# Performance work log

Hardware: AMD Instinct MI355X
Metric: run time of the kernel (lower is better)

## Reference

```python
import jax, jax.numpy as jnp
import numpy as np

B, N, E, H = 16, 1024, 128, 8  # batch, num_patches, emb_dim, num_heads
INNER = E * H                   # inner_dim = emb_dim * num_heads = 1024
LN_EPS = 1e-5
NEG_MAX = jnp.finfo(jnp.float32).max  # module uses -finfo.max on the diagonal


def setup_inputs() -> dict:
    key = jax.random.key(0)
    k0, k1, k2 = jax.random.split(key, 3)
    x = jax.random.normal(k0, (B, N, E), dtype=jnp.float32)
    ln_w = jnp.ones((E,), jnp.float32)
    ln_b = jnp.zeros((E,), jnp.float32)
    w_qkv = jax.random.normal(k1, (E, 3 * INNER), jnp.float32) * (E ** -0.5)
    scale = jnp.full((H,), E ** -0.5, jnp.float32)  # learnable per-head LSA scale
    w_proj = jax.random.normal(k2, (INNER, E), jnp.float32) * (INNER ** -0.5)
    b_proj = jnp.zeros((E,), jnp.float32)
    return {"x": x, "ln_w": ln_w, "ln_b": ln_b, "w_qkv": w_qkv,
            "scale": scale, "w_proj": w_proj, "b_proj": b_proj}


def reference(x, ln_w, ln_b, w_qkv, scale, w_proj, b_proj):
    # LayerNorm over emb_dim
    mu = jnp.mean(x, axis=-1, keepdims=True)
    var = jnp.mean(jnp.square(x - mu), axis=-1, keepdims=True)
    xn = (x - mu) * jax.lax.rsqrt(var + LN_EPS) * ln_w + ln_b

    # QKV projection (no bias), chunk into q,k,v of [B,N,INNER]
    qkv = xn @ w_qkv
    q, k, v = jnp.split(qkv, 3, axis=-1)

    # 'b n (h d) -> b h n d' with h = H, d = E
    def to_heads(t):
        return t.reshape(B, N, H, E).transpose(0, 2, 1, 3)
    q, k, v = to_heads(q), to_heads(k), to_heads(v)

    # per-head learnable scale (LSA), then mask diagonal to -max
    dots = jnp.einsum("bhnd,bhmd->bhnm", q, k) * scale[None, :, None, None]
    idx = jnp.arange(N)
    dots = dots.at[:, :, idx, idx].set(-NEG_MAX)

    attn = jax.nn.softmax(dots, axis=-1)  # dropout p=0.0 -> identity
    out = jnp.einsum("bhnm,bhmd->bhnd", attn, v)

    # 'b h n d -> b n (h d)', then output projection (with bias)
    out = out.transpose(0, 2, 1, 3).reshape(B, N, INNER)
    return out @ w_proj + b_proj
```

## Files before the change

### kernel.cpp

```cpp
#include <hip/hip_runtime.h>
#include <hip/hip_bf16.h>

typedef __bf16 bf16x8 __attribute__((ext_vector_type(8)));
typedef float f32x4 __attribute__((ext_vector_type(4)));

__device__ __forceinline__ unsigned short f2bf(float f) {
  union { __hip_bfloat16 h; unsigned short u; } cv;
  cv.h = __float2bfloat16(f);
  return cv.u;
}

__device__ __forceinline__ bf16x8 ld_frag(const unsigned short* p) {
  bf16x8 v;
  __builtin_memcpy(&v, __builtin_assume_aligned(p, 16), 16);
  return v;
}
__device__ __forceinline__ uint4 ld16(const unsigned short* p) {
  uint4 v;
  __builtin_memcpy(&v, __builtin_assume_aligned(p, 16), 16);
  return v;
}
__device__ __forceinline__ void st16(unsigned short* p, uint4 v) {
  __builtin_memcpy(__builtin_assume_aligned(p, 16), &v, 16);
}

__global__ __launch_bounds__(256) void ln_kernel(const float* __restrict__ x,
                                                 const float* __restrict__ w,
                                                 const float* __restrict__ b,
                                                 unsigned short* __restrict__ xn) {
  int wave = threadIdx.x >> 6;
  int lane = threadIdx.x & 63;
  int row = blockIdx.x * 4 + wave;
  const float* xr = x + (size_t)row * 128;
  float2 v = *reinterpret_cast<const float2*>(xr + lane * 2);
  float s1 = v.x + v.y;
  float s2 = v.x * v.x + v.y * v.y;
#pragma unroll
  for (int off = 32; off > 0; off >>= 1) {
    s1 += __shfl_xor(s1, off, 64);
    s2 += __shfl_xor(s2, off, 64);
  }
  float mu = s1 * (1.0f / 128.0f);
  float var = s2 * (1.0f / 128.0f) - mu * mu;
  float rstd = rsqrtf(var + 1e-5f);
  float a0 = (v.x - mu) * rstd * w[lane * 2] + b[lane * 2];
  float a1 = (v.y - mu) * rstd * w[lane * 2 + 1] + b[lane * 2 + 1];
  unsigned int pk = (unsigned int)f2bf(a0) | ((unsigned int)f2bf(a1) << 16);
  *reinterpret_cast<unsigned int*>(xn + (size_t)row * 128 + lane * 2) = pk;
}

__global__ __launch_bounds__(256) void tcast_kernel(const float* __restrict__ in,
                                                    unsigned short* __restrict__ out,
                                                    int R, int C) {
  __shared__ float tile[32][33];
  int tx = threadIdx.x & 31, ty = threadIdx.x >> 5;
  int c0 = blockIdx.x * 32, r0 = blockIdx.y * 32;
#pragma unroll
  for (int k = 0; k < 4; k++)
    tile[ty + 8 * k][tx] = in[(size_t)(r0 + ty + 8 * k) * C + c0 + tx];
  __syncthreads();
#pragma unroll
  for (int k = 0; k < 4; k++)
    out[(size_t)(c0 + ty + 8 * k) * R + r0 + tx] = f2bf(tile[tx][ty + 8 * k]);
}

__global__ __launch_bounds__(256) void qkv_gemm(const unsigned short* __restrict__ A,
                                                const unsigned short* __restrict__ Bt,
                                                unsigned short* __restrict__ qk,
                                                unsigned short* __restrict__ Vt) {
  __shared__ unsigned short Al[64 * 136];
  __shared__ unsigned short Bl[128 * 136];
  int t = threadIdx.x;
  int i0 = blockIdx.x * 64, c0 = blockIdx.y * 128;
  int l = t & 15, rr = t >> 4;
#pragma unroll
  for (int p = 0; p < 4; p++) {
    int r = rr + 16 * p;
    st16(&Al[r * 136 + l * 8], ld16(&A[(size_t)(i0 + r) * 128 + l * 8]));
  }
#pragma unroll
  for (int p = 0; p < 8; p++) {
    int r = rr + 16 * p;
    st16(&Bl[r * 136 + l * 8], ld16(&Bt[(size_t)(c0 + r) * 128 + l * 8]));
  }
  __syncthreads();
  int w = t >> 6, lane = t & 63, l15 = lane & 15, quad = lane >> 4;
  int wy = (w >> 1) * 32, wx = (w & 1) * 64;
  const f32x4 fz = {0.f, 0.f, 0.f, 0.f};
  f32x4 acc[2][4];
#pragma unroll
  for (int i = 0; i < 2; i++)
#pragma unroll
    for (int j = 0; j < 4; j++) acc[i][j] = fz;
#pragma unroll
  for (int ks = 0; ks < 4; ks++) {
    bf16x8 af[2], bfr[4];
#pragma unroll
    for (int i = 0; i < 2; i++)
      af[i] = ld_frag(&Al[(wy + 16 * i + l15) * 136 + 32 * ks + quad * 8]);
#pragma unroll
    for (int j = 0; j < 4; j++)
      bfr[j] = ld_frag(&Bl[(wx + 16 * j + l15) * 136 + 32 * ks + quad * 8]);
#pragma unroll
    for (int i = 0; i < 2; i++)
#pragma unroll
      for (int j = 0; j < 4; j++)
        acc[i][j] = __builtin_amdgcn_mfma_f32_16x16x32_bf16(af[i], bfr[j], acc[i][j], 0, 0, 0);
  }
  if (blockIdx.y < 16) {
#pragma unroll
    for (int i = 0; i < 2; i++)
#pragma unroll
      for (int j = 0; j < 4; j++)
#pragma unroll
        for (int r = 0; r < 4; r++) {
          int row = i0 + wy + 16 * i + quad * 4 + r;
          int col = c0 + wx + 16 * j + l15;
          qk[(size_t)row * 2048 + col] = f2bf(acc[i][j][r]);
        }
  } else {
    int vc0 = (blockIdx.y - 16) * 128;
#pragma unroll
    for (int i = 0; i < 2; i++)
#pragma unroll
      for (int j = 0; j < 4; j++) {
        int vcol = vc0 + wx + 16 * j + l15;
        int hh = vcol >> 7, dd = vcol & 127;
        int row0 = i0 + wy + 16 * i + quad * 4;
        int bb = row0 >> 10, nn = row0 & 1023;
        ushort4 pk;
        pk.x = f2bf(acc[i][j][0]); pk.y = f2bf(acc[i][j][1]);
        pk.z = f2bf(acc[i][j][2]); pk.w = f2bf(acc[i][j][3]);
        *reinterpret_cast<ushort4*>(Vt + (size_t)(bb * 8 + hh) * 131072 +
                                    (size_t)dd * 1024 + nn) = pk;
      }
  }
}

__global__ __launch_bounds__(256, 3) void attn_kernel(const unsigned short* __restrict__ qk,
                                                      const unsigned short* __restrict__ Vt,
                                                      const float* __restrict__ scale,
                                                      unsigned short* __restrict__ aout) {
  __shared__ unsigned short Kl[64 * 136];
  __shared__ unsigned short Vl[128 * 72];
  __shared__ unsigned short Pl[128 * 72];
  int t = threadIdx.x;
  int idx = blockIdx.x;
  int bh = idx & 127, qt = idx >> 7;
  int b = bh >> 3, h = bh & 7;
  int q0 = qt * 128;
  float sc = scale[h];
  int w = t >> 6, lane = t & 63, l15 = lane & 15, quad = lane >> 4;

  bf16x8 qf[2][4];
#pragma unroll
  for (int g = 0; g < 2; g++) {
    const unsigned short* qp =
        qk + (size_t)(b * 1024 + q0 + 32 * w + 16 * g + l15) * 2048 + h * 128;
#pragma unroll
    for (int ks = 0; ks < 4; ks++) qf[g][ks] = ld_frag(qp + 32 * ks + quad * 8);
  }
  const f32x4 fz = {0.f, 0.f, 0.f, 0.f};
  f32x4 o[2][8];
#pragma unroll
  for (int g = 0; g < 2; g++)
#pragma unroll
    for (int i = 0; i < 8; i++) o[g][i] = fz;
  float plsum[2][4];
#pragma unroll
  for (int g = 0; g < 2; g++)
#pragma unroll
    for (int r = 0; r < 4; r++) plsum[g][r] = 0.f;

  const unsigned short* kbase = qk + (size_t)b * 1024 * 2048 + 1024 + h * 128;
  const unsigned short* vbase = Vt + (size_t)bh * 131072;
  int lk = t & 15, rrk = t >> 4;
  int lv = t & 7, rrv = t >> 3;

  for (int kt = 0; kt < 16; kt++) {
    int k0 = kt * 64;
    uint4 kreg[4], vreg[4];
#pragma unroll
    for (int p = 0; p < 4; p++)
      kreg[p] = ld16(kbase + (size_t)(k0 + rrk + 16 * p) * 2048 + lk * 8);
#pragma unroll
    for (int p = 0; p < 4; p++)
      vreg[p] = ld16(vbase + (size_t)(rrv + 32 * p) * 1024 + k0 + lv * 8);
    __syncthreads();
#pragma unroll
    for (int p = 0; p < 4; p++) st16(&Kl[(rrk + 16 * p) * 136 + lk * 8], kreg[p]);
#pragma unroll
    for (int p = 0; p < 4; p++) st16(&Vl[(rrv + 32 * p) * 72 + lv * 8], vreg[p]);
    __syncthreads();

#pragma unroll
    for (int ct = 0; ct < 4; ct++) {
      f32x4 acc0 = fz, acc1 = fz;
#pragma unroll
      for (int ks = 0; ks < 4; ks++) {
        bf16x8 kf = ld_frag(&Kl[(16 * ct + l15) * 136 + 32 * ks + quad * 8]);
        acc0 = __builtin_amdgcn_mfma_f32_16x16x32_bf16(qf[0][ks], kf, acc0, 0, 0, 0);
        acc1 = __builtin_amdgcn_mfma_f32_16x16x32_bf16(qf[1][ks], kf, acc1, 0, 0, 0);
      }
#pragma unroll
      for (int g = 0; g < 2; g++) {
        f32x4 a = g ? acc1 : acc0;
        bool dj = (q0 + 32 * w + 16 * g) == (k0 + 16 * ct);
#pragma unroll
        for (int r = 0; r < 4; r++) {
          float p = __expf(a[r] * sc);
          if (dj && (quad * 4 + r) == l15) p = 0.f;
          plsum[g][r] += p;
          Pl[(32 * w + 16 * g + quad * 4 + r) * 72 + 16 * ct + l15] = f2bf(p);
        }
      }
    }
    __syncthreads();

    bf16x8 pa[2][2];
#pragma unroll
    for (int g = 0; g < 2; g++)
#pragma unroll
      for (int ks2 = 0; ks2 < 2; ks2++)
        pa[g][ks2] = ld_frag(&Pl[(32 * w + 16 * g + l15) * 72 + 32 * ks2 + quad * 8]);
#pragma unroll
    for (int c8 = 0; c8 < 8; c8++) {
#pragma unroll
      for (int ks2 = 0; ks2 < 2; ks2++) {
        bf16x8 vf = ld_frag(&Vl[(16 * c8 + l15) * 72 + 32 * ks2 + quad * 8]);
        o[0][c8] = __builtin_amdgcn_mfma_f32_16x16x32_bf16(pa[0][ks2], vf, o[0][c8], 0, 0, 0);
        o[1][c8] = __builtin_amdgcn_mfma_f32_16x16x32_bf16(pa[1][ks2], vf, o[1][c8], 0, 0, 0);
      }
    }
  }

#pragma unroll
  for (int g = 0; g < 2; g++)
#pragma unroll
    for (int r = 0; r < 4; r++) {
      float s = plsum[g][r];
#pragma unroll
      for (int off = 1; off < 16; off <<= 1) s += __shfl_xor(s, off, 64);
      float rl = 1.0f / s;
      int row = b * 1024 + q0 + 32 * w + 16 * g + quad * 4 + r;
#pragma unroll
      for (int c8 = 0; c8 < 8; c8++) {
        int col = h * 128 + 16 * c8 + l15;
        aout[(size_t)row * 1024 + col] = f2bf(o[g][c8][r] * rl);
      }
    }
}

__global__ __launch_bounds__(256) void proj_gemm(const unsigned short* __restrict__ A,
                                                 const unsigned short* __restrict__ Bt,
                                                 const float* __restrict__ bias,
                                                 float* __restrict__ out) {
  __shared__ unsigned short Al[64 * 136];
  __shared__ unsigned short Bl[128 * 136];
  int t = threadIdx.x;
  int i0 = blockIdx.x * 64;
  int w = t >> 6, lane = t & 63, l15 = lane & 15, quad = lane >> 4;
  int wy = (w >> 1) * 32, wx = (w & 1) * 64;
  const f32x4 fz = {0.f, 0.f, 0.f, 0.f};
  f32x4 acc[2][4];
#pragma unroll
  for (int i = 0; i < 2; i++)
#pragma unroll
    for (int j = 0; j < 4; j++) acc[i][j] = fz;
  int l = t & 15, rr = t >> 4;
  for (int kb = 0; kb < 8; kb++) {
    int k0 = kb * 128;
    uint4 areg[4], breg[8];
#pragma unroll
    for (int p = 0; p < 4; p++)
      areg[p] = ld16(&A[(size_t)(i0 + rr + 16 * p) * 1024 + k0 + l * 8]);
#pragma unroll
    for (int p = 0; p < 8; p++)
      breg[p] = ld16(&Bt[(size_t)(rr + 16 * p) * 1024 + k0 + l * 8]);
    __syncthreads();
#pragma unroll
    for (int p = 0; p < 4; p++) st16(&Al[(rr + 16 * p) * 136 + l * 8], areg[p]);
#pragma unroll
    for (int p = 0; p < 8; p++) st16(&Bl[(rr + 16 * p) * 136 + l * 8], breg[p]);
    __syncthreads();
#pragma unroll
    for (int ks = 0; ks < 4; ks++) {
      bf16x8 af[2], bfr[4];
#pragma unroll
      for (int i = 0; i < 2; i++)
        af[i] = ld_frag(&Al[(wy + 16 * i + l15) * 136 + 32 * ks + quad * 8]);
#pragma unroll
      for (int j = 0; j < 4; j++)
        bfr[j] = ld_frag(&Bl[(wx + 16 * j + l15) * 136 + 32 * ks + quad * 8]);
#pragma unroll
      for (int i = 0; i < 2; i++)
#pragma unroll
        for (int j = 0; j < 4; j++)
          acc[i][j] = __builtin_amdgcn_mfma_f32_16x16x32_bf16(af[i], bfr[j], acc[i][j], 0, 0, 0);
    }
  }
#pragma unroll
  for (int i = 0; i < 2; i++)
#pragma unroll
    for (int j = 0; j < 4; j++) {
      int col = wx + 16 * j + l15;
      float bv = bias[col];
#pragma unroll
      for (int r = 0; r < 4; r++) {
        int row = i0 + wy + 16 * i + quad * 4 + r;
        out[(size_t)row * 128 + col] = acc[i][j][r] + bv;
      }
    }
}

extern "C" void kernel_launch(void* const* d_in, const int* in_sizes, int n_in,
                              void* d_out, int out_size, void* d_ws, size_t ws_size,
                              hipStream_t stream) {
  const float* x      = (const float*)d_in[0];
  const float* ln_w   = (const float*)d_in[1];
  const float* ln_b   = (const float*)d_in[2];
  const float* w_qkv  = (const float*)d_in[3];
  const float* scale  = (const float*)d_in[4];
  const float* w_proj = (const float*)d_in[5];
  const float* b_proj = (const float*)d_in[6];
  float* out = (float*)d_out;

  char* ws = (char*)d_ws;
  unsigned short* xn     = (unsigned short*)(ws);
  unsigned short* wqkvT  = (unsigned short*)(ws + 4194304);
  unsigned short* wprojT = (unsigned short*)(ws + 4980736);
  unsigned short* qk     = (unsigned short*)(ws + 5242880);
  unsigned short* Vt     = (unsigned short*)(ws + 72351744);
  unsigned short* aout   = (unsigned short*)(ws + 105906176);

  ln_kernel<<<dim3(4096), dim3(256), 0, stream>>>(x, ln_w, ln_b, xn);
  tcast_kernel<<<dim3(96, 4), dim3(256), 0, stream>>>(w_qkv, wqkvT, 128, 3072);
  tcast_kernel<<<dim3(4, 32), dim3(256), 0, stream>>>(w_proj, wprojT, 1024, 128);
  qkv_gemm<<<dim3(256, 24), dim3(256), 0, stream>>>(xn, wqkvT, qk, Vt);
  attn_kernel<<<dim3(1024), dim3(256), 0, stream>>>(qk, Vt, scale, aout);
  proj_gemm<<<dim3(256), dim3(256), 0, stream>>>(aout, wprojT, b_proj, out);
}
```

Baseline: 216.1 us.

## Retile QKV, attention and projection kernels; read K/V fragments directly from global

The QKV GEMM moves to 128x128 tiles with K split into two 64-wide LDS stages. The attention kernel now processes 256 queries per block, 64 per wave, and drops the shared K/V staging and block-wide barriers. Each wave loads K and V MFMA fragments straight from global or L2 and writes P into its own swizzled LDS slice. The projection GEMM is split into two 64-column halves to double the grid. Together these aim for more reuse per block and less synchronisation, at the cost of higher register pressure, lower occupancy (launch bound 2) and uncoalesced-looking global fragment loads.

```diff
diff --git a/kernel.cpp b/kernel.cpp
--- a/kernel.cpp
+++ b/kernel.cpp
@@ -68,48 +68,55 @@
                                                 const unsigned short* __restrict__ Bt,
                                                 unsigned short* __restrict__ qk,
                                                 unsigned short* __restrict__ Vt) {
-  __shared__ unsigned short Al[64 * 136];
-  __shared__ unsigned short Bl[128 * 136];
+  __shared__ unsigned short Al[128 * 72];
+  __shared__ unsigned short Bl[128 * 72];
   int t = threadIdx.x;
-  int i0 = blockIdx.x * 64, c0 = blockIdx.y * 128;
-  int l = t & 15, rr = t >> 4;
-#pragma unroll
-  for (int p = 0; p < 4; p++) {
-    int r = rr + 16 * p;
-    st16(&Al[r * 136 + l * 8], ld16(&A[(size_t)(i0 + r) * 128 + l * 8]));
-  }
-#pragma unroll
-  for (int p = 0; p < 8; p++) {
-    int r = rr + 16 * p;
-    st16(&Bl[r * 136 + l * 8], ld16(&Bt[(size_t)(c0 + r) * 128 + l * 8]));
-  }
-  __syncthreads();
+  int i0 = blockIdx.x * 128, c0 = blockIdx.y * 128;
+  int lg = t & 7, rr = t >> 3;
   int w = t >> 6, lane = t & 63, l15 = lane & 15, quad = lane >> 4;
-  int wy = (w >> 1) * 32, wx = (w & 1) * 64;
+  int wy = (w >> 1) * 64, wx = (w & 1) * 64;
   const f32x4 fz = {0.f, 0.f, 0.f, 0.f};
-  f32x4 acc[2][4];
-#pragma unroll
-  for (int i = 0; i < 2; i++)
+  f32x4 acc[4][4];
+#pragma unroll
+  for (int i = 0; i < 4; i++)
 #pragma unroll
     for (int j = 0; j < 4; j++) acc[i][j] = fz;
-#pragma unroll
-  for (int ks = 0; ks < 4; ks++) {
-    bf16x8 af[2], bfr[4];
-#pragma unroll
-    for (int i = 0; i < 2; i++)
-      af[i] = ld_frag(&Al[(wy + 16 * i + l15) * 136 + 32 * ks + quad * 8]);
-#pragma unroll
-    for (int j = 0; j < 4; j++)
-      bfr[j] = ld_frag(&Bl[(wx + 16 * j + l15) * 136 + 32 * ks + quad * 8]);
-#pragma unroll
-    for (int i = 0; i < 2; i++)
+
+#pragma unroll
+  for (int kt = 0; kt < 2; kt++) {
+    int k0 = kt * 64;
+    uint4 areg[4], breg[4];
+#pragma unroll
+    for (int p = 0; p < 4; p++)
+      areg[p] = ld16(&A[(size_t)(i0 + rr + 32 * p) * 128 + k0 + lg * 8]);
+#pragma unroll
+    for (int p = 0; p < 4; p++)
+      breg[p] = ld16(&Bt[(size_t)(c0 + rr + 32 * p) * 128 + k0 + lg * 8]);
+    __syncthreads();
+#pragma unroll
+    for (int p = 0; p < 4; p++) st16(&Al[(rr + 32 * p) * 72 + lg * 8], areg[p]);
+#pragma unroll
+    for (int p = 0; p < 4; p++) st16(&Bl[(rr + 32 * p) * 72 + lg * 8], breg[p]);
+    __syncthreads();
+#pragma unroll
+    for (int ks = 0; ks < 2; ks++) {
+      bf16x8 af[4], bfr[4];
+#pragma unroll
+      for (int i = 0; i < 4; i++)
+        af[i] = ld_frag(&Al[(wy + 16 * i + l15) * 72 + 32 * ks + quad * 8]);
 #pragma unroll
       for (int j = 0; j < 4; j++)
-        acc[i][j] = __builtin_amdgcn_mfma_f32_16x16x32_bf16(af[i], bfr[j], acc[i][j], 0, 0, 0);
+        bfr[j] = ld_frag(&Bl[(wx + 16 * j + l15) * 72 + 32 * ks + quad * 8]);
+#pragma unroll
+      for (int i = 0; i < 4; i++)
+#pragma unroll
+        for (int j = 0; j < 4; j++)
+          acc[i][j] = __builtin_amdgcn_mfma_f32_16x16x32_bf16(af[i], bfr[j], acc[i][j], 0, 0, 0);
+    }
   }
   if (blockIdx.y < 16) {
 #pragma unroll
-    for (int i = 0; i < 2; i++)
+    for (int i = 0; i < 4; i++)
 #pragma unroll
       for (int j = 0; j < 4; j++)
 #pragma unroll
@@ -121,7 +128,7 @@
   } else {
     int vc0 = (blockIdx.y - 16) * 128;
 #pragma unroll
-    for (int i = 0; i < 2; i++)
+    for (int i = 0; i < 4; i++)
 #pragma unroll
       for (int j = 0; j < 4; j++) {
         int vcol = vc0 + wx + 16 * j + l15;
@@ -137,112 +144,100 @@
   }
 }
 
-__global__ __launch_bounds__(256, 3) void attn_kernel(const unsigned short* __restrict__ qk,
+__global__ __launch_bounds__(256, 2) void attn_kernel(const unsigned short* __restrict__ qk,
                                                       const unsigned short* __restrict__ Vt,
                                                       const float* __restrict__ scale,
                                                       unsigned short* __restrict__ aout) {
-  __shared__ unsigned short Kl[64 * 136];
-  __shared__ unsigned short Vl[128 * 72];
-  __shared__ unsigned short Pl[128 * 72];
+  __shared__ unsigned short Pl[256 * 72];
   int t = threadIdx.x;
   int idx = blockIdx.x;
   int bh = idx & 127, qt = idx >> 7;
   int b = bh >> 3, h = bh & 7;
-  int q0 = qt * 128;
+  int q0 = qt * 256;
   float sc = scale[h];
   int w = t >> 6, lane = t & 63, l15 = lane & 15, quad = lane >> 4;
 
-  bf16x8 qf[2][4];
-#pragma unroll
-  for (int g = 0; g < 2; g++) {
-    const unsigned short* qp =
-        qk + (size_t)(b * 1024 + q0 + 32 * w + 16 * g + l15) * 2048 + h * 128;
-#pragma unroll
-    for (int ks = 0; ks < 4; ks++) qf[g][ks] = ld_frag(qp + 32 * ks + quad * 8);
+  bf16x8 qf[4][4];
+  {
+    const unsigned short* qb = qk + (size_t)(b * 1024) * 2048 + h * 128;
+#pragma unroll
+    for (int g = 0; g < 4; g++) {
+      const unsigned short* qp = qb + (size_t)(q0 + 64 * w + 16 * g + l15) * 2048;
+#pragma unroll
+      for (int ks = 0; ks < 4; ks++) qf[g][ks] = ld_frag(qp + 32 * ks + quad * 8);
+    }
   }
   const f32x4 fz = {0.f, 0.f, 0.f, 0.f};
-  f32x4 o[2][8];
-#pragma unroll
-  for (int g = 0; g < 2; g++)
+  f32x4 o[4][8];
+#pragma unroll
+  for (int g = 0; g < 4; g++)
 #pragma unroll
     for (int i = 0; i < 8; i++) o[g][i] = fz;
-  float plsum[2][4];
-#pragma unroll
-  for (int g = 0; g < 2; g++)
+  float plsum[4][4];
+#pragma unroll
+  for (int g = 0; g < 4; g++)
 #pragma unroll
     for (int r = 0; r < 4; r++) plsum[g][r] = 0.f;
 
-  const unsigned short* kbase = qk + (size_t)b * 1024 * 2048 + 1024 + h * 128;
+  const unsigned short* kbase = qk + (size_t)(b * 1024) * 2048 + 1024 + h * 128;
   const unsigned short* vbase = Vt + (size_t)bh * 131072;
-  int lk = t & 15, rrk = t >> 4;
-  int lv = t & 7, rrv = t >> 3;
+  unsigned short* Pw = &Pl[(64 * w) * 72];
+  int rswz = (l15 >> 2) << 1;
+  int wgoff = ((2 * 0) + 0, 0);
+  (void)wgoff;
 
   for (int kt = 0; kt < 16; kt++) {
     int k0 = kt * 64;
-    uint4 kreg[4], vreg[4];
-#pragma unroll
-    for (int p = 0; p < 4; p++)
-      kreg[p] = ld16(kbase + (size_t)(k0 + rrk + 16 * p) * 2048 + lk * 8);
-#pragma unroll
-    for (int p = 0; p < 4; p++)
-      vreg[p] = ld16(vbase + (size_t)(rrv + 32 * p) * 1024 + k0 + lv * 8);
-    __syncthreads();
-#pragma unroll
-    for (int p = 0; p < 4; p++) st16(&Kl[(rrk + 16 * p) * 136 + lk * 8], kreg[p]);
-#pragma unroll
-    for (int p = 0; p < 4; p++) st16(&Vl[(rrv + 32 * p) * 72 + lv * 8], vreg[p]);
-    __syncthreads();
-
 #pragma unroll
     for (int ct = 0; ct < 4; ct++) {
-      f32x4 acc0 = fz, acc1 = fz;
+      f32x4 acc[4] = {fz, fz, fz, fz};
 #pragma unroll
       for (int ks = 0; ks < 4; ks++) {
-        bf16x8 kf = ld_frag(&Kl[(16 * ct + l15) * 136 + 32 * ks + quad * 8]);
-        acc0 = __builtin_amdgcn_mfma_f32_16x16x32_bf16(qf[0][ks], kf, acc0, 0, 0, 0);
-        acc1 = __builtin_amdgcn_mfma_f32_16x16x32_bf16(qf[1][ks], kf, acc1, 0, 0, 0);
-      }
-#pragma unroll
-      for (int g = 0; g < 2; g++) {
-        f32x4 a = g ? acc1 : acc0;
-        bool dj = (q0 + 32 * w + 16 * g) == (k0 + 16 * ct);
+        bf16x8 kf = ld_frag(kbase + (size_t)(k0 + 16 * ct + l15) * 2048 + 32 * ks + quad * 8);
+#pragma unroll
+        for (int g = 0; g < 4; g++)
+          acc[g] = __builtin_amdgcn_mfma_f32_16x16x32_bf16(qf[g][ks], kf, acc[g], 0, 0, 0);
+      }
+      int wg = (((2 * ct + (l15 >> 3)) ^ (quad << 1)) << 3) + (l15 & 7);
+#pragma unroll
+      for (int g = 0; g < 4; g++) {
+        bool dj = (q0 + 64 * w + 16 * g) == (k0 + 16 * ct);
 #pragma unroll
         for (int r = 0; r < 4; r++) {
-          float p = __expf(a[r] * sc);
+          float p = __expf(acc[g][r] * sc);
           if (dj && (quad * 4 + r) == l15) p = 0.f;
           plsum[g][r] += p;
-          Pl[(32 * w + 16 * g + quad * 4 + r) * 72 + 16 * ct + l15] = f2bf(p);
+          Pw[(16 * g + quad * 4 + r) * 72 + wg] = f2bf(p);
         }
       }
     }
-    __syncthreads();
-
-    bf16x8 pa[2][2];
-#pragma unroll
-    for (int g = 0; g < 2; g++)
+    bf16x8 pa[4][2];
+#pragma unroll
+    for (int g = 0; g < 4; g++)
 #pragma unroll
       for (int ks2 = 0; ks2 < 2; ks2++)
-        pa[g][ks2] = ld_frag(&Pl[(32 * w + 16 * g + l15) * 72 + 32 * ks2 + quad * 8]);
+        pa[g][ks2] = ld_frag(&Pw[(16 * g + l15) * 72 + (((4 * ks2 + quad) ^ rswz) << 3)]);
 #pragma unroll
     for (int c8 = 0; c8 < 8; c8++) {
 #pragma unroll
       for (int ks2 = 0; ks2 < 2; ks2++) {
-        bf16x8 vf = ld_frag(&Vl[(16 * c8 + l15) * 72 + 32 * ks2 + quad * 8]);
-        o[0][c8] = __builtin_amdgcn_mfma_f32_16x16x32_bf16(pa[0][ks2], vf, o[0][c8], 0, 0, 0);
-        o[1][c8] = __builtin_amdgcn_mfma_f32_16x16x32_bf16(pa[1][ks2], vf, o[1][c8], 0, 0, 0);
-      }
-    }
-  }
-
-#pragma unroll
-  for (int g = 0; g < 2; g++)
+        bf16x8 vf = ld_frag(vbase + (size_t)(16 * c8 + l15) * 1024 + k0 + 32 * ks2 + quad * 8);
+#pragma unroll
+        for (int g = 0; g < 4; g++)
+          o[g][c8] = __builtin_amdgcn_mfma_f32_16x16x32_bf16(pa[g][ks2], vf, o[g][c8], 0, 0, 0);
+      }
+    }
+  }
+
+#pragma unroll
+  for (int g = 0; g < 4; g++)
 #pragma unroll
     for (int r = 0; r < 4; r++) {
       float s = plsum[g][r];
 #pragma unroll
       for (int off = 1; off < 16; off <<= 1) s += __shfl_xor(s, off, 64);
       float rl = 1.0f / s;
-      int row = b * 1024 + q0 + 32 * w + 16 * g + quad * 4 + r;
+      int row = b * 1024 + q0 + 64 * w + 16 * g + quad * 4 + r;
 #pragma unroll
       for (int c8 = 0; c8 < 8; c8++) {
         int col = h * 128 + 16 * c8 + l15;
@@ -256,54 +251,54 @@
                                                  const float* __restrict__ bias,
                                                  float* __restrict__ out) {
   __shared__ unsigned short Al[64 * 136];
-  __shared__ unsigned short Bl[128 * 136];
+  __shared__ unsigned short Bl[64 * 136];
   int t = threadIdx.x;
-  int i0 = blockIdx.x * 64;
+  int i0 = blockIdx.x * 64, c0 = blockIdx.y * 64;
   int w = t >> 6, lane = t & 63, l15 = lane & 15, quad = lane >> 4;
-  int wy = (w >> 1) * 32, wx = (w & 1) * 64;
+  int wy = (w >> 1) * 32, wx = (w & 1) * 32;
   const f32x4 fz = {0.f, 0.f, 0.f, 0.f};
-  f32x4 acc[2][4];
+  f32x4 acc[2][2];
 #pragma unroll
   for (int i = 0; i < 2; i++)
 #pragma unroll
-    for (int j = 0; j < 4; j++) acc[i][j] = fz;
+    for (int j = 0; j < 2; j++) acc[i][j] = fz;
   int l = t & 15, rr = t >> 4;
   for (int kb = 0; kb < 8; kb++) {
     int k0 = kb * 128;
-    uint4 areg[4], breg[8];
+    uint4 areg[4], breg[4];
 #pragma unroll
     for (int p = 0; p < 4; p++)
       areg[p] = ld16(&A[(size_t)(i0 + rr + 16 * p) * 1024 + k0 + l * 8]);
 #pragma unroll
-    for (int p = 0; p < 8; p++)
-      breg[p] = ld16(&Bt[(size_t)(rr + 16 * p) * 1024 + k0 + l * 8]);
+    for (int p = 0; p < 4; p++)
+      breg[p] = ld16(&Bt[(size_t)(c0 + rr + 16 * p) * 1024 + k0 + l * 8]);
     __syncthreads();
 #pragma unroll
     for (int p = 0; p < 4; p++) st16(&Al[(rr + 16 * p) * 136 + l * 8], areg[p]);
 #pragma unroll
-    for (int p = 0; p < 8; p++) st16(&Bl[(rr + 16 * p) * 136 + l * 8], breg[p]);
+    for (int p = 0; p < 4; p++) st16(&Bl[(rr + 16 * p) * 136 + l * 8], breg[p]);
     __syncthreads();
 #pragma unroll
     for (int ks = 0; ks < 4; ks++) {
-      bf16x8 af[2], bfr[4];
+      bf16x8 af[2], bfr[2];
 #pragma unroll
       for (int i = 0; i < 2; i++)
         af[i] = ld_frag(&Al[(wy + 16 * i + l15) * 136 + 32 * ks + quad * 8]);
 #pragma unroll
-      for (int j = 0; j < 4; j++)
+      for (int j = 0; j < 2; j++)
         bfr[j] = ld_frag(&Bl[(wx + 16 * j + l15) * 136 + 32 * ks + quad * 8]);
 #pragma unroll
       for (int i = 0; i < 2; i++)
 #pragma unroll
-        for (int j = 0; j < 4; j++)
+        for (int j = 0; j < 2; j++)
           acc[i][j] = __builtin_amdgcn_mfma_f32_16x16x32_bf16(af[i], bfr[j], acc[i][j], 0, 0, 0);
     }
   }
 #pragma unroll
   for (int i = 0; i < 2; i++)
 #pragma unroll
-    for (int j = 0; j < 4; j++) {
-      int col = wx + 16 * j + l15;
+    for (int j = 0; j < 2; j++) {
+      int col = c0 + wx + 16 * j + l15;
       float bv = bias[col];
 #pragma unroll
       for (int r = 0; r < 4; r++) {
@@ -336,7 +331,7 @@
   ln_kernel<<<dim3(4096), dim3(256), 0, stream>>>(x, ln_w, ln_b, xn);
   tcast_kernel<<<dim3(96, 4), dim3(256), 0, stream>>>(w_qkv, wqkvT, 128, 3072);
   tcast_kernel<<<dim3(4, 32), dim3(256), 0, stream>>>(w_proj, wprojT, 1024, 128);
-  qkv_gemm<<<dim3(256, 24), dim3(256), 0, stream>>>(xn, wqkvT, qk, Vt);
-  attn_kernel<<<dim3(1024), dim3(256), 0, stream>>>(qk, Vt, scale, aout);
-  proj_gemm<<<dim3(256), dim3(256), 0, stream>>>(aout, wprojT, b_proj, out);
-}
+  qkv_gemm<<<dim3(128, 24), dim3(256), 0, stream>>>(xn, wqkvT, qk, Vt);
+  attn_kernel<<<dim3(512), dim3(256), 0, stream>>>(qk, Vt, scale, aout);
+  proj_gemm<<<dim3(256, 2), dim3(256), 0, stream>>>(aout, wprojT, b_proj, out);
+}
```

New measurement: 298.9 us. +38.3%, slower.
